# Kernel optimization log

Measured on AMD Instinct MI355X. Metric: run time of the kernel, lower is better.

## Reference

```python
import jax, jax.numpy as jnp
import numpy as np

IN_DIM, HID, MID, FFN, OUT = 384, 128, 1024, 512, 1024
B, T = 8, 4096
LN_EPS = 1e-5


def _legs_hippo(n: int) -> np.ndarray:
    # A[i, j] = P_i(2j/n - 1) * sqrt(2i + 1), Legendre via 3-term recurrence
    x = 2.0 * np.arange(n) / n - 1.0          # eval points, shape [n]
    P = np.zeros((n, n), dtype=np.float64)     # P[i] = P_i(x)
    P[0] = 1.0
    if n > 1:
        P[1] = x
    for i in range(1, n - 1):
        P[i + 1] = ((2 * i + 1) * x * P[i] - i * P[i - 1]) / (i + 1)
    A = P * np.sqrt(2.0 * np.arange(n) + 1.0)[:, None]
    # rescale so the 4096-step recurrence stays finite (A is a free Parameter,
    # so any test value is valid; unscaled LegS overflows fp32 in ~20 steps)
    s = np.linalg.norm(A, 2)
    return (A / (1.05 * s)).astype(np.float32)


def _layernorm(x, g, b):
    mu = jnp.mean(x, axis=-1, keepdims=True)
    var = jnp.var(x, axis=-1, keepdims=True)
    return (x - mu) * jax.lax.rsqrt(var + LN_EPS) * g + b


def setup_inputs() -> dict:
    key = jax.random.key(0)
    ks = jax.random.split(key, 16)

    def w(k, shape, fan_in):
        return jax.random.normal(k, shape, jnp.float32) * (1.0 / np.sqrt(fan_in))

    return {
        "padded_x": jax.random.normal(ks[0], (B, T, IN_DIM), jnp.float32),
        "seq_lens": jax.random.randint(ks[1], (B,), 1, T + 1, jnp.int32),
        "A": jnp.asarray(_legs_hippo(HID)),
        "enc_w1": w(ks[2], (IN_DIM, MID), IN_DIM), "enc_b1": jnp.zeros((MID,), jnp.float32),
        "enc_w2": w(ks[3], (MID, HID), MID), "enc_b2": jnp.zeros((HID,), jnp.float32),
        "proj_w": w(ks[4], (HID, MID), HID), "proj_b": jnp.zeros((MID,), jnp.float32),
        "ln1_g": jnp.ones((MID,), jnp.float32), "ln1_b": jnp.zeros((MID,), jnp.float32),
        "ffn_w1": w(ks[5], (MID, FFN), MID), "ffn_b1": jnp.zeros((FFN,), jnp.float32),
        "ffn_w2": w(ks[6], (FFN, OUT), FFN), "ffn_b2": jnp.zeros((OUT,), jnp.float32),
        "ln2_g": jnp.ones((OUT,), jnp.float32), "ln2_b": jnp.zeros((OUT,), jnp.float32),
        "out_w": w(ks[7], (OUT, OUT), OUT), "out_b": jnp.zeros((OUT,), jnp.float32),
    }


def reference(padded_x, seq_lens, A, enc_w1, enc_b1, enc_w2, enc_b2,
              proj_w, proj_b, ln1_g, ln1_b, ffn_w1, ffn_b1, ffn_w2, ffn_b2,
              ln2_g, ln2_b, out_w, out_b):
    # encoder: Linear -> GELU(exact) -> Linear   [B, T, HID]
    h_mid = jax.nn.gelu(padded_x @ enc_w1 + enc_b1, approximate=False)
    seqs_bx = h_mid @ enc_w2 + enc_b2

    # masked linear recurrence h_t = A @ h_{t-1} + Bx_t via lax.scan over time
    xs = jnp.swapaxes(seqs_bx, 0, 1)           # [T, B, HID]
    ts = jnp.arange(xs.shape[0])

    def step(h, inp):
        x_t, t = inp
        upd = h @ A.T + x_t                     # (A @ h)^T batched
        mask = (t < seq_lens)[:, None]          # [B, 1]
        return jnp.where(mask, upd, h), None

    h0 = jnp.zeros((padded_x.shape[0], A.shape[0]), padded_x.dtype)
    batch_h, _ = jax.lax.scan(step, h0, (xs, ts))

    # decoder
    projected = batch_h @ proj_w + proj_b
    norm_h = _layernorm(projected, ln1_g, ln1_b)
    ffn_out = jax.nn.gelu(norm_h @ ffn_w1 + ffn_b1, approximate=False) @ ffn_w2 + ffn_b2
    ffn_out = ffn_out + projected               # residual (requires OUT == MID)
    norm_ffn = _layernorm(ffn_out, ln2_g, ln2_b)
    return norm_ffn @ out_w + out_b             # [B, OUT]
```

## Files before the change

kernel.cpp:

```cpp
#include <hip/hip_runtime.h>

typedef __attribute__((ext_vector_type(8))) short short8;
typedef __attribute__((ext_vector_type(4))) short short4v;
typedef __attribute__((ext_vector_type(4))) float float4v;

__device__ __forceinline__ float bf2f(short s) {
  union { float f; unsigned u; } cv; cv.u = ((unsigned)(unsigned short)s) << 16; return cv.f;
}
__device__ __forceinline__ short f2bf(float f) {
  union { float f; unsigned u; } cv; cv.f = f;
  unsigned u = cv.u;
  unsigned r = u + 0x7FFFu + ((u >> 16) & 1u);
  return (short)(r >> 16);
}
__device__ __forceinline__ float gelu_f(float v) {
  return 0.5f * v * (1.0f + erff(v * 0.70710678118654752440f));
}
__device__ __forceinline__ void glds16(const short* g, short* l) {
  __builtin_amdgcn_global_load_lds(
      (const __attribute__((address_space(1))) void*)g,
      (__attribute__((address_space(3))) void*)l, 16, 0, 0);
}

template<int EPI>
__global__ __launch_bounds__(256) void gemm_bt(
    const short* __restrict__ A_, const short* __restrict__ BT,
    const float* __restrict__ bias, void* __restrict__ out,
    int lda, int ldb, int ldc, int kSteps, int kChunk,
    const int* __restrict__ seq_lens, int seqSkip)
{
  int m0 = blockIdx.y * 128;
  int n0 = blockIdx.x * 128;
  if (seqSkip) {
    int b = m0 >> 12, t = m0 & 4095;
    if (t >= seq_lens[b]) return;
  }
  int kBase = blockIdx.z * kChunk;

  __shared__ __align__(16) short As[128 * 64];
  __shared__ __align__(16) short Bs[128 * 64];

  int tid = threadIdx.x;
  int lane = tid & 63, wave = tid >> 6;
  int l15 = lane & 15, quad = lane >> 4;
  int wm = wave & 1, wn = wave >> 1;
  int lr = lane >> 3, lseg = lane & 7;

  float4v acc[4][4];
#pragma unroll
  for (int i = 0; i < 4; i++)
#pragma unroll
    for (int j = 0; j < 4; j++) acc[i][j] = 0;

  for (int ks = 0; ks < kSteps; ++ks) {
    int kk = kBase + ks * 64;
#pragma unroll
    for (int i = 0; i < 4; i++) {
      int rowg = wave * 32 + i * 8;
      glds16(A_ + (size_t)(m0 + rowg + lr) * lda + kk + lseg * 8, &As[rowg * 64]);
      glds16(BT + (size_t)(n0 + rowg + lr) * ldb + kk + lseg * 8, &Bs[rowg * 64]);
    }
    __syncthreads();
#pragma unroll
    for (int kh = 0; kh < 2; kh++) {
      short8 af[4], bfr[4];
#pragma unroll
      for (int im = 0; im < 4; im++)
        af[im] = *(short8*)&As[(wm * 64 + im * 16 + l15) * 64 + kh * 32 + quad * 8];
#pragma unroll
      for (int in = 0; in < 4; in++)
        bfr[in] = *(short8*)&Bs[(wn * 64 + in * 16 + l15) * 64 + kh * 32 + quad * 8];
#pragma unroll
      for (int im = 0; im < 4; im++)
#pragma unroll
        for (int in = 0; in < 4; in++)
          acc[im][in] = __builtin_amdgcn_mfma_f32_16x16x32_bf16(af[im], bfr[in], acc[im][in], 0, 0, 0);
    }
    __syncthreads();
  }

#pragma unroll
  for (int im = 0; im < 4; im++) {
#pragma unroll
    for (int in = 0; in < 4; in++) {
      int n = n0 + wn * 64 + in * 16 + l15;
#pragma unroll
      for (int reg = 0; reg < 4; reg++) {
        int m = m0 + wm * 64 + im * 16 + quad * 4 + reg;
        float v = acc[im][in][reg];
        if (EPI == 0) {
          v += bias[n]; v = gelu_f(v);
          ((short*)out)[(size_t)m * ldc + n] = f2bf(v);
        } else if (EPI == 1) {
          v += bias[n];
          ((short*)out)[(size_t)m * ldc + n] = f2bf(v);
        } else {
          atomicAdd((float*)out + (size_t)m * ldc + n, v);
        }
      }
    }
  }
}

__global__ void prep_wide(const float* __restrict__ x, const float* __restrict__ w1,
                          const float* __restrict__ w2,
                          const float* __restrict__ proj_w, const float* __restrict__ ffn_w1,
                          const float* __restrict__ ffn_w2, const float* __restrict__ out_w,
                          const float* __restrict__ A,
                          short* __restrict__ xB,
                          short* __restrict__ w1T, short* __restrict__ w2T,
                          short* __restrict__ projB, short* __restrict__ ffn1B,
                          short* __restrict__ ffn2B, short* __restrict__ outB,
                          short* __restrict__ P1, short* __restrict__ P1t,
                          short* __restrict__ P2t,
                          short* __restrict__ Spow, short* __restrict__ SpowT)
{
  int idx = blockIdx.x * 256 + threadIdx.x;
  if (idx < 3145728) {
    float4v v = ((const float4v*)x)[idx];
    short4v o;
#pragma unroll
    for (int j = 0; j < 4; j++) o[j] = f2bf(v[j]);
    ((short4v*)xB)[idx] = o;
    return;
  }
  idx -= 3145728;
  if (idx < 393216) {
    int n = idx / 384, k = idx % 384;
    w1T[idx] = f2bf(w1[k * 1024 + n]);
    return;
  }
  idx -= 393216;
  if (idx < 131072) {
    int n = idx / 1024, k = idx % 1024;
    w2T[idx] = f2bf(w2[k * 128 + n]);
    return;
  }
  idx -= 131072;
  if (idx < 131072) { projB[idx] = f2bf(proj_w[idx]); return; }
  idx -= 131072;
  if (idx < 524288) { ffn1B[idx] = f2bf(ffn_w1[idx]); return; }
  idx -= 524288;
  if (idx < 524288) { ffn2B[idx] = f2bf(ffn_w2[idx]); return; }
  idx -= 524288;
  if (idx < 1048576) { outB[idx] = f2bf(out_w[idx]); return; }
  idx -= 1048576;
  if (idx < 16384) {
    int i = idx >> 7, j = idx & 127;
    short bidv = f2bf((i == j) ? 1.0f : 0.0f);
    P1[i * 8192 + 63 * 128 + j] = bidv;
    P1t[(63 * 128 + j) * 128 + i] = bidv;
    P2t[(63 * 128 + j) * 128 + i] = bidv;
    short ab = f2bf(A[idx]);
    Spow[idx] = ab;
    SpowT[(size_t)j * 128 + i] = ab;
  }
}

__global__ __launch_bounds__(256) void pow_chain(short* __restrict__ Spow,
                                                 short* __restrict__ SpowT)
{
  __shared__ short X[16384];
  __shared__ short XT[16384];
  int t = threadIdx.x;
  for (int i = t * 8; i < 16384; i += 2048) {
    *(short8*)&X[i]  = *(const short8*)&Spow[i];
    *(short8*)&XT[i] = *(const short8*)&SpowT[i];
  }
  __syncthreads();
  int lane = t & 63, wave = t >> 6, l15 = lane & 15, quad = lane >> 4;
  for (int step = 1; step <= 11; ++step) {
    short8 af[2][4], bfr[8][4];
#pragma unroll
    for (int mt = 0; mt < 2; mt++)
#pragma unroll
      for (int ks = 0; ks < 4; ks++)
        af[mt][ks] = *(short8*)&X[(wave * 32 + mt * 16 + l15) * 128 + ks * 32 + quad * 8];
#pragma unroll
    for (int nt = 0; nt < 8; nt++)
#pragma unroll
      for (int ks = 0; ks < 4; ks++)
        bfr[nt][ks] = *(short8*)&XT[(nt * 16 + l15) * 128 + ks * 32 + quad * 8];
    __syncthreads();
    float4v acc[2][8];
#pragma unroll
    for (int mt = 0; mt < 2; mt++)
#pragma unroll
      for (int nt = 0; nt < 8; nt++) acc[mt][nt] = 0;
#pragma unroll
    for (int ks = 0; ks < 4; ks++)
#pragma unroll
      for (int mt = 0; mt < 2; mt++)
#pragma unroll
        for (int nt = 0; nt < 8; nt++)
          acc[mt][nt] = __builtin_amdgcn_mfma_f32_16x16x32_bf16(af[mt][ks], bfr[nt][ks], acc[mt][nt], 0, 0, 0);
    short* gX  = Spow  + (size_t)step * 16384;
    short* gXT = SpowT + (size_t)step * 16384;
#pragma unroll
    for (int mt = 0; mt < 2; mt++)
#pragma unroll
      for (int nt = 0; nt < 8; nt++)
#pragma unroll
        for (int reg = 0; reg < 4; reg++) {
          int m = wave * 32 + mt * 16 + quad * 4 + reg;
          int n = nt * 16 + l15;
          short v = f2bf(acc[mt][nt][reg]);
          X[m * 128 + n] = v; XT[n * 128 + m] = v;
          gX[m * 128 + n] = v; gXT[n * 128 + m] = v;
        }
    __syncthreads();
  }
}

__global__ __launch_bounds__(256) void pow_fill(const short* __restrict__ Spow,
                                                const short* __restrict__ SpowT,
                                                short* __restrict__ P1,
                                                short* __restrict__ P1t,
                                                short* __restrict__ P2t)
{
  __shared__ short cur[16384];
  __shared__ short Bt[16384];
  int bid = blockIdx.x;
  int table1 = bid < 63;
  int e = table1 ? bid + 1 : bid - 62;
  int t = threadIdx.x;
  int lane = t & 63, wave = t >> 6, l15 = lane & 15, quad = lane >> 4;

  int bits = e;
  int k0 = __ffs(bits) - 1; bits &= bits - 1;
  int s0 = table1 ? k0 : (k0 == 0 ? 6 : 6 + k0);
  for (int i = t * 8; i < 16384; i += 2048)
    *(short8*)&cur[i] = *(const short8*)&Spow[(size_t)s0 * 16384 + i];

  while (bits) {
    int k = __ffs(bits) - 1; bits &= bits - 1;
    int si = table1 ? k : (k == 0 ? 6 : 6 + k);
    for (int i = t * 8; i < 16384; i += 2048)
      *(short8*)&Bt[i] = *(const short8*)&SpowT[(size_t)si * 16384 + i];
    __syncthreads();
    short8 af[2][4], bfr[8][4];
#pragma unroll
    for (int mt = 0; mt < 2; mt++)
#pragma unroll
      for (int ks = 0; ks < 4; ks++)
        af[mt][ks] = *(short8*)&cur[(wave * 32 + mt * 16 + l15) * 128 + ks * 32 + quad * 8];
#pragma unroll
    for (int nt = 0; nt < 8; nt++)
#pragma unroll
      for (int ks = 0; ks < 4; ks++)
        bfr[nt][ks] = *(short8*)&Bt[(nt * 16 + l15) * 128 + ks * 32 + quad * 8];
    __syncthreads();
    float4v acc[2][8];
#pragma unroll
    for (int mt = 0; mt < 2; mt++)
#pragma unroll
      for (int nt = 0; nt < 8; nt++) acc[mt][nt] = 0;
#pragma unroll
    for (int ks = 0; ks < 4; ks++)
#pragma unroll
      for (int mt = 0; mt < 2; mt++)
#pragma unroll
        for (int nt = 0; nt < 8; nt++)
          acc[mt][nt] = __builtin_amdgcn_mfma_f32_16x16x32_bf16(af[mt][ks], bfr[nt][ks], acc[mt][nt], 0, 0, 0);
#pragma unroll
    for (int mt = 0; mt < 2; mt++)
#pragma unroll
      for (int nt = 0; nt < 8; nt++)
#pragma unroll
        for (int reg = 0; reg < 4; reg++) {
          int m = wave * 32 + mt * 16 + quad * 4 + reg;
          int n = nt * 16 + l15;
          cur[m * 128 + n] = f2bf(acc[mt][nt][reg]);
        }
    __syncthreads();
  }
  __syncthreads();
  int slot = 63 - e;
  for (int idx = t; idx < 16384; idx += 256) {
    int i = idx >> 7, j = idx & 127;
    short v = cur[idx];
    if (table1) {
      P1[i * 8192 + slot * 128 + j] = v;
      P1t[(slot * 128 + j) * 128 + i] = v;
    } else {
      P2t[(slot * 128 + j) * 128 + i] = v;
    }
  }
}

__global__ void build_shift(const float* __restrict__ V, const short* __restrict__ seqs,
                            const int* __restrict__ seq_lens,
                            short* __restrict__ Vsh, short* __restrict__ TlX)
{
  int idx = blockIdx.x * 256 + threadIdx.x;
  int pp = idx >> 16;
  int e = idx & 65535;
  int k = e >> 3, b = e & 7;
  int cp = k >> 7, i = k & 127;
  int L = seq_lens[b];
  short v = 0;
  if (pp == 0) {
    int F = L >> 6;
    int sh = 64 - F;
    if (cp >= sh) v = f2bf(V[(size_t)(b * 64 + (cp - sh)) * 128 + i]);
    Vsh[e] = v;
  } else {
    int F = L >> 6, rr = L & 63;
    int sh = 64 - rr;
    if (cp >= sh) v = seqs[((size_t)b * 4096 + F * 64 + (cp - sh)) * 128 + i];
    TlX[e] = v;
  }
}

__global__ __launch_bounds__(256) void tiny_gemm(
    const short* __restrict__ Vsh, const short* __restrict__ TlX,
    const short* __restrict__ P2t, const short* __restrict__ P1t,
    float* __restrict__ hFtail)
{
  int pp = blockIdx.x >> 4, ks = blockIdx.x & 15;
  const short* X = pp ? TlX : Vsh;
  const short* P = pp ? P1t : P2t;
  float* outp = hFtail + pp * 1024;
  int i = threadIdx.x & 127, g = threadIdx.x >> 7;
  float acc[4] = {0, 0, 0, 0};
  for (int k = ks * 512; k < ks * 512 + 512; ++k) {
    float pv = bf2f(P[k * 128 + i]);
    short4v xv = *(const short4v*)(X + k * 8 + g * 4);
#pragma unroll
    for (int q = 0; q < 4; q++) acc[q] += bf2f(xv[q]) * pv;
  }
#pragma unroll
  for (int q = 0; q < 4; q++) atomicAdd(&outp[(g * 4 + q) * 128 + i], acc[q]);
}

__global__ __launch_bounds__(256) void proj_stage(
    const float* __restrict__ hFtail, const short* __restrict__ P1t,
    const int* __restrict__ seq_lens, const short* __restrict__ projB,
    const float* __restrict__ proj_b, float* __restrict__ projected)
{
  __shared__ short hT[128 * 8];
  __shared__ float red[4][64][8];
  int t = threadIdx.x;
  {
    int b = t >> 5, i4 = (t & 31) * 4;
    int rr = seq_lens[b] & 63;
    const short* M = P1t + (size_t)(63 - rr) * 128 * 128;
    const float* hF = hFtail + b * 128;
    float acc[4];
#pragma unroll
    for (int q = 0; q < 4; q++) acc[q] = hFtail[1024 + b * 128 + i4 + q];
    for (int j = 0; j < 128; ++j) {
      float hv = hF[j];
      short4v mv = *(const short4v*)&M[j * 128 + i4];
#pragma unroll
      for (int q = 0; q < 4; q++) acc[q] += bf2f(mv[q]) * hv;
    }
#pragma unroll
    for (int q = 0; q < 4; q++) hT[(i4 + q) * 8 + b] = f2bf(acc[q]);
  }
  __syncthreads();
  int c = t & 63, sl = t >> 6;
  int n = blockIdx.x * 64 + c;
  float acc[8] = {0, 0, 0, 0, 0, 0, 0, 0};
  for (int k = sl * 32; k < sl * 32 + 32; ++k) {
    short8 xv = *(short8*)&hT[k * 8];
    float wv = bf2f(projB[k * 1024 + n]);
#pragma unroll
    for (int b = 0; b < 8; b++) acc[b] += bf2f(xv[b]) * wv;
  }
#pragma unroll
  for (int b = 0; b < 8; b++) red[sl][c][b] = acc[b];
  __syncthreads();
  if (sl == 0) {
#pragma unroll
    for (int s = 1; s < 4; s++)
#pragma unroll
      for (int b = 0; b < 8; b++) acc[b] += red[s][c][b];
    float bn = proj_b[n];
#pragma unroll
    for (int b = 0; b < 8; b++) projected[b * 1024 + n] = acc[b] + bn;
  }
}

__global__ __launch_bounds__(256) void ffn1_stage(
    const float* __restrict__ projected, const float* __restrict__ g1,
    const float* __restrict__ b1, const short* __restrict__ ffn1B,
    float* __restrict__ ffn1raw)
{
  __shared__ float part[8][32][2];
  __shared__ float stats[8][2];
  __shared__ short xT[256 * 8];
  __shared__ float red[4][64][8];
  int t = threadIdx.x;
  { int b = t >> 5, j0 = t & 31; float s = 0, q = 0;
    for (int k = j0 * 32; k < j0 * 32 + 32; ++k) { float v = projected[b * 1024 + k]; s += v; q += v * v; }
    part[b][j0][0] = s; part[b][j0][1] = q; }
  __syncthreads();
  if (t < 8) {
    float s = 0, q = 0;
    for (int j = 0; j < 32; j++) { s += part[t][j][0]; q += part[t][j][1]; }
    float mu = s * (1.0f / 1024.0f);
    float var = q * (1.0f / 1024.0f) - mu * mu;
    stats[t][0] = mu; stats[t][1] = rsqrtf(var + 1e-5f);
  }
  __syncthreads();
  int ky0 = blockIdx.y * 256;
  for (int idx = t; idx < 2048; idx += 256) {
    int kl = idx >> 3, b = idx & 7; int k = ky0 + kl;
    float v = (projected[b * 1024 + k] - stats[b][0]) * stats[b][1] * g1[k] + b1[k];
    xT[kl * 8 + b] = f2bf(v);
  }
  __syncthreads();
  int c = t & 63, sl = t >> 6;
  int n = blockIdx.x * 64 + c;
  float acc[8] = {0, 0, 0, 0, 0, 0, 0, 0};
  for (int kl = sl * 64; kl < sl * 64 + 64; ++kl) {
    short8 xv = *(short8*)&xT[kl * 8];
    float wv = bf2f(ffn1B[(size_t)(ky0 + kl) * 512 + n]);
#pragma unroll
    for (int b = 0; b < 8; b++) acc[b] += bf2f(xv[b]) * wv;
  }
#pragma unroll
  for (int b = 0; b < 8; b++) red[sl][c][b] = acc[b];
  __syncthreads();
  if (sl == 0) {
#pragma unroll
    for (int s = 1; s < 4; s++)
#pragma unroll
      for (int b = 0; b < 8; b++) acc[b] += red[s][c][b];
#pragma unroll
    for (int b = 0; b < 8; b++) atomicAdd(&ffn1raw[b * 512 + n], acc[b]);
  }
}

__global__ __launch_bounds__(256) void ffn2_stage(
    const float* __restrict__ ffn1raw, const float* __restrict__ fb1,
    const short* __restrict__ ffn2B, float* __restrict__ ffn2raw)
{
  __shared__ short xT[256 * 8];
  __shared__ float red[4][64][8];
  int t = threadIdx.x;
  int ky0 = blockIdx.y * 256;
  for (int idx = t; idx < 2048; idx += 256) {
    int kl = idx >> 3, b = idx & 7; int k = ky0 + kl;
    float v = gelu_f(ffn1raw[b * 512 + k] + fb1[k]);
    xT[kl * 8 + b] = f2bf(v);
  }
  __syncthreads();
  int c = t & 63, sl = t >> 6;
  int n = blockIdx.x * 64 + c;
  float acc[8] = {0, 0, 0, 0, 0, 0, 0, 0};
  for (int kl = sl * 64; kl < sl * 64 + 64; ++kl) {
    short8 xv = *(short8*)&xT[kl * 8];
    float wv = bf2f(ffn2B[(size_t)(ky0 + kl) * 1024 + n]);
#pragma unroll
    for (int b = 0; b < 8; b++) acc[b] += bf2f(xv[b]) * wv;
  }
#pragma unroll
  for (int b = 0; b < 8; b++) red[sl][c][b] = acc[b];
  __syncthreads();
  if (sl == 0) {
#pragma unroll
    for (int s = 1; s < 4; s++)
#pragma unroll
      for (int b = 0; b < 8; b++) acc[b] += red[s][c][b];
#pragma unroll
    for (int b = 0; b < 8; b++) atomicAdd(&ffn2raw[b * 1024 + n], acc[b]);
  }
}

__global__ __launch_bounds__(256) void out_stage(
    const float* __restrict__ ffn2raw, const float* __restrict__ fb2,
    const float* __restrict__ projected, const float* __restrict__ g2,
    const float* __restrict__ b2ln, const short* __restrict__ outB,
    const float* __restrict__ out_b, float* __restrict__ d_out)
{
  __shared__ float part[8][32][2];
  __shared__ float stats[8][2];
  __shared__ short xT[512 * 8];
  __shared__ float red[4][64][8];
  int t = threadIdx.x;
  { int b = t >> 5, j0 = t & 31; float s = 0, q = 0;
    for (int k = j0 * 32; k < j0 * 32 + 32; ++k) {
      float v = ffn2raw[b * 1024 + k] + fb2[k] + projected[b * 1024 + k];
      s += v; q += v * v;
    }
    part[b][j0][0] = s; part[b][j0][1] = q; }
  __syncthreads();
  if (t < 8) {
    float s = 0, q = 0;
    for (int j = 0; j < 32; j++) { s += part[t][j][0]; q += part[t][j][1]; }
    float mu = s * (1.0f / 1024.0f);
    float var = q * (1.0f / 1024.0f) - mu * mu;
    stats[t][0] = mu; stats[t][1] = rsqrtf(var + 1e-5f);
  }
  __syncthreads();
  int ky0 = blockIdx.y * 512;
  for (int idx = t; idx < 4096; idx += 256) {
    int kl = idx >> 3, b = idx & 7; int k = ky0 + kl;
    float v = ffn2raw[b * 1024 + k] + fb2[k] + projected[b * 1024 + k];
    v = (v - stats[b][0]) * stats[b][1] * g2[k] + b2ln[k];
    xT[kl * 8 + b] = f2bf(v);
  }
  __syncthreads();
  int c = t & 63, sl = t >> 6;
  int n = blockIdx.x * 64 + c;
  float acc[8] = {0, 0, 0, 0, 0, 0, 0, 0};
  for (int kl = sl * 128; kl < sl * 128 + 128; ++kl) {
    short8 xv = *(short8*)&xT[kl * 8];
    float wv = bf2f(outB[(size_t)(ky0 + kl) * 1024 + n]);
#pragma unroll
    for (int b = 0; b < 8; b++) acc[b] += bf2f(xv[b]) * wv;
  }
#pragma unroll
  for (int b = 0; b < 8; b++) red[sl][c][b] = acc[b];
  __syncthreads();
  if (sl == 0) {
#pragma unroll
    for (int s = 1; s < 4; s++)
#pragma unroll
      for (int b = 0; b < 8; b++) acc[b] += red[s][c][b];
    float bn = (blockIdx.y == 0) ? out_b[n] : 0.0f;
#pragma unroll
    for (int b = 0; b < 8; b++) atomicAdd(&d_out[b * 1024 + n], acc[b] + bn);
  }
}

extern "C" void kernel_launch(void* const* d_in, const int* in_sizes, int n_in,
                              void* d_out, int out_size, void* d_ws, size_t ws_size,
                              hipStream_t stream)
{
  (void)in_sizes; (void)n_in; (void)out_size; (void)ws_size;
  const float* x      = (const float*)d_in[0];
  const int* seq_lens = (const int*)d_in[1];
  const float* A      = (const float*)d_in[2];
  const float* enc_w1 = (const float*)d_in[3];
  const float* enc_b1 = (const float*)d_in[4];
  const float* enc_w2 = (const float*)d_in[5];
  const float* enc_b2 = (const float*)d_in[6];
  const float* proj_w = (const float*)d_in[7];
  const float* proj_b = (const float*)d_in[8];
  const float* ln1_g  = (const float*)d_in[9];
  const float* ln1_b  = (const float*)d_in[10];
  const float* ffn_w1 = (const float*)d_in[11];
  const float* ffn_b1 = (const float*)d_in[12];
  const float* ffn_w2 = (const float*)d_in[13];
  const float* ffn_b2 = (const float*)d_in[14];
  const float* ln2_g  = (const float*)d_in[15];
  const float* ln2_b  = (const float*)d_in[16];
  const float* out_w  = (const float*)d_in[17];
  const float* out_b  = (const float*)d_in[18];

  char* p = (char*)d_ws;
  auto alloc = [&](size_t bytes) { char* r = p; p += (bytes + 255) & ~(size_t)255; return r; };
  short* h_mid = (short*)alloc(32768ull * 1024 * 2);
  short* xB    = (short*)alloc(32768ull * 384 * 2);
  short* seqs  = (short*)alloc(32768ull * 128 * 2);
  short* w1T   = (short*)alloc(1024ull * 384 * 2);
  short* w2T   = (short*)alloc(128ull * 1024 * 2);
  short* projB = (short*)alloc(128ull * 1024 * 2);
  short* ffn1B = (short*)alloc(1024ull * 512 * 2);
  short* ffn2B = (short*)alloc(512ull * 1024 * 2);
  short* outB  = (short*)alloc(1024ull * 1024 * 2);
  short* Spow  = (short*)alloc(12ull * 16384 * 2);
  short* SpowT = (short*)alloc(12ull * 16384 * 2);
  short* P1    = (short*)alloc(128ull * 8192 * 2);
  short* P1t   = (short*)alloc(8192ull * 128 * 2);
  short* P2t   = (short*)alloc(8192ull * 128 * 2);
  float* V       = (float*)alloc(512ull * 128 * 4);
  float* hFtail  = (float*)alloc(2ull * 8 * 128 * 4);
  float* ffn1raw = (float*)alloc(8ull * 512 * 4);
  float* ffn2raw = (float*)alloc(8ull * 1024 * 4);
  short* Vsh   = (short*)alloc(8192ull * 8 * 2);
  short* TlX   = (short*)alloc(8192ull * 8 * 2);
  float* projected = (float*)alloc(8ull * 1024 * 4);

  hipMemsetAsync(V, 0, (512ull * 128 + 2ull * 8 * 128 + 8ull * 512 + 8ull * 1024) * 4, stream);
  hipMemsetAsync(d_out, 0, 8192ull * 4, stream);

  prep_wide<<<23104, 256, 0, stream>>>(x, enc_w1, enc_w2, proj_w, ffn_w1, ffn_w2, out_w, A,
      xB, w1T, w2T, projB, ffn1B, ffn2B, outB, P1, P1t, P2t, Spow, SpowT);
  pow_chain<<<1, 256, 0, stream>>>(Spow, SpowT);
  pow_fill<<<126, 256, 0, stream>>>(Spow, SpowT, P1, P1t, P2t);

  gemm_bt<0><<<dim3(8, 256, 1), 256, 0, stream>>>(xB, w1T, enc_b1, h_mid,
      384, 384, 1024, 6, 0, seq_lens, 1);
  gemm_bt<1><<<dim3(1, 256, 1), 256, 0, stream>>>(h_mid, w2T, enc_b2, seqs,
      1024, 1024, 128, 16, 0, seq_lens, 1);

  gemm_bt<2><<<dim3(1, 4, 16), 256, 0, stream>>>(seqs, P1, nullptr, V,
      8192, 8192, 128, 8, 512, seq_lens, 0);
  build_shift<<<512, 256, 0, stream>>>(V, seqs, seq_lens, Vsh, TlX);
  tiny_gemm<<<32, 256, 0, stream>>>(Vsh, TlX, P2t, P1t, hFtail);

  proj_stage<<<16, 256, 0, stream>>>(hFtail, P1t, seq_lens, projB, proj_b, projected);
  ffn1_stage<<<dim3(8, 4), 256, 0, stream>>>(projected, ln1_g, ln1_b, ffn1B, ffn1raw);
  ffn2_stage<<<dim3(16, 2), 256, 0, stream>>>(ffn1raw, ffn_b1, ffn2B, ffn2raw);
  out_stage<<<dim3(16, 2), 256, 0, stream>>>(ffn2raw, ffn_b2, projected, ln2_g, ln2_b,
      outB, out_b, (float*)d_out);
}
```

Baseline: 441.1 us.

## Fuse encoder GEMMs, swizzle LDS, replace atomics with split-K partials

```diff
diff --git a/kernel.cpp b/kernel.cpp
--- a/kernel.cpp
+++ b/kernel.cpp
@@ -22,19 +22,143 @@
       (__attribute__((address_space(3))) void*)l, 16, 0, 0);
 }
 
-template<int EPI>
+__global__ __launch_bounds__(256) void enc_fused(
+    const short* __restrict__ xB, const short* __restrict__ w1T,
+    const short* __restrict__ w2T, const float* __restrict__ b1,
+    const float* __restrict__ b2, short* __restrict__ seqs,
+    const int* __restrict__ seq_lens)
+{
+  int m0 = blockIdx.x * 64;
+  { int b = m0 >> 12, t = m0 & 4095; if (t >= seq_lens[b]) return; }
+
+  __shared__ __align__(16) short As[64 * 64];
+  __shared__ __align__(16) short Ws[128 * 64];
+  __shared__ __align__(16) short midb[64 * 128];
+
+  int tid = threadIdx.x, lane = tid & 63, wave = tid >> 6;
+  int l15 = lane & 15, quad = lane >> 4;
+  int lr = lane >> 3, lseg = lane & 7;
+
+  float4v accO[4][2];
+#pragma unroll
+  for (int i = 0; i < 4; i++)
+#pragma unroll
+    for (int j = 0; j < 2; j++) accO[i][j] = 0;
+
+  for (int nc = 0; nc < 8; ++nc) {
+    float4v accM[4][2];
+#pragma unroll
+    for (int i = 0; i < 4; i++)
+#pragma unroll
+      for (int j = 0; j < 2; j++) accM[i][j] = 0;
+
+    for (int ks = 0; ks < 6; ++ks) {
+      int kk = ks * 64;
+#pragma unroll
+      for (int i = 0; i < 2; i++) {
+        int rowg = wave * 16 + i * 8;
+        glds16(xB + (size_t)(m0 + rowg + lr) * 384 + kk + (lseg ^ lr) * 8, &As[rowg * 64]);
+      }
+#pragma unroll
+      for (int i = 0; i < 4; i++) {
+        int rowg = wave * 32 + i * 8;
+        glds16(w1T + (size_t)(nc * 128 + rowg + lr) * 384 + kk + (lseg ^ lr) * 8, &Ws[rowg * 64]);
+      }
+      __syncthreads();
+#pragma unroll
+      for (int kh = 0; kh < 2; kh++) {
+        int s = kh * 4 + quad;
+        short8 af[4], bfr[2];
+#pragma unroll
+        for (int im = 0; im < 4; im++) {
+          int r = im * 16 + l15;
+          af[im] = *(short8*)&As[r * 64 + ((s ^ (r & 7)) * 8)];
+        }
+#pragma unroll
+        for (int in = 0; in < 2; in++) {
+          int r = wave * 32 + in * 16 + l15;
+          bfr[in] = *(short8*)&Ws[r * 64 + ((s ^ (r & 7)) * 8)];
+        }
+#pragma unroll
+        for (int im = 0; im < 4; im++)
+#pragma unroll
+          for (int in = 0; in < 2; in++)
+            accM[im][in] = __builtin_amdgcn_mfma_f32_16x16x32_bf16(af[im], bfr[in], accM[im][in], 0, 0, 0);
+      }
+      __syncthreads();
+    }
+#pragma unroll
+    for (int im = 0; im < 4; im++)
+#pragma unroll
+      for (int in = 0; in < 2; in++) {
+        int k = wave * 32 + in * 16 + l15;
+        float bias = b1[nc * 128 + k];
+#pragma unroll
+        for (int reg = 0; reg < 4; reg++) {
+          int m = im * 16 + quad * 4 + reg;
+          float v = gelu_f(accM[im][in][reg] + bias);
+          int s = k >> 3;
+          int sw = (s & 8) | ((s & 7) ^ (m & 7));
+          midb[m * 128 + sw * 8 + (k & 7)] = f2bf(v);
+        }
+      }
+    __syncthreads();
+#pragma unroll
+    for (int ks2 = 0; ks2 < 2; ++ks2) {
+      int kk = nc * 128 + ks2 * 64;
+#pragma unroll
+      for (int i = 0; i < 4; i++) {
+        int rowg = wave * 32 + i * 8;
+        glds16(w2T + (size_t)(rowg + lr) * 1024 + kk + (lseg ^ lr) * 8, &Ws[rowg * 64]);
+      }
+      __syncthreads();
+#pragma unroll
+      for (int kh = 0; kh < 2; kh++) {
+        short8 af[4], bfr[2];
+#pragma unroll
+        for (int im = 0; im < 4; im++) {
+          int m = im * 16 + l15;
+          int kb = ks2 * 64 + kh * 32 + quad * 8;
+          int s = kb >> 3;
+          int sw = (s & 8) | ((s & 7) ^ (m & 7));
+          af[im] = *(short8*)&midb[m * 128 + sw * 8];
+        }
+#pragma unroll
+        for (int in = 0; in < 2; in++) {
+          int r = wave * 32 + in * 16 + l15;
+          int s = kh * 4 + quad;
+          bfr[in] = *(short8*)&Ws[r * 64 + ((s ^ (r & 7)) * 8)];
+        }
+#pragma unroll
+        for (int im = 0; im < 4; im++)
+#pragma unroll
+          for (int in = 0; in < 2; in++)
+            accO[im][in] = __builtin_amdgcn_mfma_f32_16x16x32_bf16(af[im], bfr[in], accO[im][in], 0, 0, 0);
+      }
+      __syncthreads();
+    }
+  }
+#pragma unroll
+  for (int im = 0; im < 4; im++)
+#pragma unroll
+    for (int in = 0; in < 2; in++) {
+      int n = wave * 32 + in * 16 + l15;
+      float bias = b2[n];
+#pragma unroll
+      for (int reg = 0; reg < 4; reg++) {
+        int m = m0 + im * 16 + quad * 4 + reg;
+        seqs[(size_t)m * 128 + n] = f2bf(accO[im][in][reg] + bias);
+      }
+    }
+}
+
 __global__ __launch_bounds__(256) void gemm_bt(
     const short* __restrict__ A_, const short* __restrict__ BT,
-    const float* __restrict__ bias, void* __restrict__ out,
-    int lda, int ldb, int ldc, int kSteps, int kChunk,
-    const int* __restrict__ seq_lens, int seqSkip)
+    float* __restrict__ out, int lda, int ldb, int ldc,
+    int kSteps, int kChunk)
 {
   int m0 = blockIdx.y * 128;
   int n0 = blockIdx.x * 128;
-  if (seqSkip) {
-    int b = m0 >> 12, t = m0 & 4095;
-    if (t >= seq_lens[b]) return;
-  }
   int kBase = blockIdx.z * kChunk;
 
   __shared__ __align__(16) short As[128 * 64];
@@ -57,19 +181,24 @@
 #pragma unroll
     for (int i = 0; i < 4; i++) {
       int rowg = wave * 32 + i * 8;
-      glds16(A_ + (size_t)(m0 + rowg + lr) * lda + kk + lseg * 8, &As[rowg * 64]);
-      glds16(BT + (size_t)(n0 + rowg + lr) * ldb + kk + lseg * 8, &Bs[rowg * 64]);
+      glds16(A_ + (size_t)(m0 + rowg + lr) * lda + kk + (lseg ^ lr) * 8, &As[rowg * 64]);
+      glds16(BT + (size_t)(n0 + rowg + lr) * ldb + kk + (lseg ^ lr) * 8, &Bs[rowg * 64]);
     }
     __syncthreads();
 #pragma unroll
     for (int kh = 0; kh < 2; kh++) {
+      int s = kh * 4 + quad;
       short8 af[4], bfr[4];
 #pragma unroll
-      for (int im = 0; im < 4; im++)
-        af[im] = *(short8*)&As[(wm * 64 + im * 16 + l15) * 64 + kh * 32 + quad * 8];
-#pragma unroll
-      for (int in = 0; in < 4; in++)
-        bfr[in] = *(short8*)&Bs[(wn * 64 + in * 16 + l15) * 64 + kh * 32 + quad * 8];
+      for (int im = 0; im < 4; im++) {
+        int r = wm * 64 + im * 16 + l15;
+        af[im] = *(short8*)&As[r * 64 + ((s ^ (r & 7)) * 8)];
+      }
+#pragma unroll
+      for (int in = 0; in < 4; in++) {
+        int r = wn * 64 + in * 16 + l15;
+        bfr[in] = *(short8*)&Bs[r * 64 + ((s ^ (r & 7)) * 8)];
+      }
 #pragma unroll
       for (int im = 0; im < 4; im++)
 #pragma unroll
@@ -78,28 +207,18 @@
     }
     __syncthreads();
   }
-
-#pragma unroll
-  for (int im = 0; im < 4; im++) {
+  float* outz = out + (size_t)blockIdx.z * 65536;
+#pragma unroll
+  for (int im = 0; im < 4; im++)
 #pragma unroll
     for (int in = 0; in < 4; in++) {
       int n = n0 + wn * 64 + in * 16 + l15;
 #pragma unroll
       for (int reg = 0; reg < 4; reg++) {
         int m = m0 + wm * 64 + im * 16 + quad * 4 + reg;
-        float v = acc[im][in][reg];
-        if (EPI == 0) {
-          v += bias[n]; v = gelu_f(v);
-          ((short*)out)[(size_t)m * ldc + n] = f2bf(v);
-        } else if (EPI == 1) {
-          v += bias[n];
-          ((short*)out)[(size_t)m * ldc + n] = f2bf(v);
-        } else {
-          atomicAdd((float*)out + (size_t)m * ldc + n, v);
-        }
-      }
-    }
-  }
+        outz[(size_t)m * ldc + n] = acc[im][in][reg];
+      }
+    }
 }
 
 __global__ void prep_wide(const float* __restrict__ x, const float* __restrict__ w1,
@@ -288,44 +407,44 @@
   }
 }
 
-__global__ void build_shift(const float* __restrict__ V, const short* __restrict__ seqs,
-                            const int* __restrict__ seq_lens,
-                            short* __restrict__ Vsh, short* __restrict__ TlX)
-{
-  int idx = blockIdx.x * 256 + threadIdx.x;
-  int pp = idx >> 16;
-  int e = idx & 65535;
-  int k = e >> 3, b = e & 7;
-  int cp = k >> 7, i = k & 127;
-  int L = seq_lens[b];
-  short v = 0;
-  if (pp == 0) {
-    int F = L >> 6;
-    int sh = 64 - F;
-    if (cp >= sh) v = f2bf(V[(size_t)(b * 64 + (cp - sh)) * 128 + i]);
-    Vsh[e] = v;
-  } else {
-    int F = L >> 6, rr = L & 63;
-    int sh = 64 - rr;
-    if (cp >= sh) v = seqs[((size_t)b * 4096 + F * 64 + (cp - sh)) * 128 + i];
-    TlX[e] = v;
-  }
-}
-
-__global__ __launch_bounds__(256) void tiny_gemm(
-    const short* __restrict__ Vsh, const short* __restrict__ TlX,
+__global__ __launch_bounds__(256) void combine_gemm(
+    const float* __restrict__ Vz, const short* __restrict__ seqs,
+    const int* __restrict__ seq_lens,
     const short* __restrict__ P2t, const short* __restrict__ P1t,
     float* __restrict__ hFtail)
 {
+  __shared__ short X[512 * 8];
   int pp = blockIdx.x >> 4, ks = blockIdx.x & 15;
-  const short* X = pp ? TlX : Vsh;
+  int t = threadIdx.x;
+  for (int e = t; e < 4096; e += 256) {
+    int klocal = e >> 3, b = e & 7;
+    int cp = ks * 4 + (klocal >> 7), i = klocal & 127;
+    int L = seq_lens[b];
+    if (pp == 0) {
+      int F = L >> 6, sh = 64 - F;
+      float v = 0.f;
+      if (cp >= sh) {
+        int row = (b * 64 + (cp - sh)) * 128 + i;
+#pragma unroll
+        for (int z = 0; z < 16; z++) v += Vz[(size_t)z * 65536 + row];
+      }
+      X[e] = f2bf(v);
+    } else {
+      int F = L >> 6, rr = L & 63, sh = 64 - rr;
+      short s = 0;
+      if (cp >= sh) s = seqs[((size_t)b * 4096 + F * 64 + (cp - sh)) * 128 + i];
+      X[e] = s;
+    }
+  }
+  __syncthreads();
   const short* P = pp ? P1t : P2t;
   float* outp = hFtail + pp * 1024;
-  int i = threadIdx.x & 127, g = threadIdx.x >> 7;
+  int i = t & 127, g = t >> 7;
   float acc[4] = {0, 0, 0, 0};
-  for (int k = ks * 512; k < ks * 512 + 512; ++k) {
+  for (int kl = 0; kl < 512; ++kl) {
+    int k = ks * 512 + kl;
     float pv = bf2f(P[k * 128 + i]);
-    short4v xv = *(const short4v*)(X + k * 8 + g * 4);
+    short4v xv = *(const short4v*)(X + kl * 8 + g * 4);
 #pragma unroll
     for (int q = 0; q < 4; q++) acc[q] += bf2f(xv[q]) * pv;
   }
@@ -553,7 +672,6 @@
 
   char* p = (char*)d_ws;
   auto alloc = [&](size_t bytes) { char* r = p; p += (bytes + 255) & ~(size_t)255; return r; };
-  short* h_mid = (short*)alloc(32768ull * 1024 * 2);
   short* xB    = (short*)alloc(32768ull * 384 * 2);
   short* seqs  = (short*)alloc(32768ull * 128 * 2);
   short* w1T   = (short*)alloc(1024ull * 384 * 2);
@@ -567,15 +685,13 @@
   short* P1    = (short*)alloc(128ull * 8192 * 2);
   short* P1t   = (short*)alloc(8192ull * 128 * 2);
   short* P2t   = (short*)alloc(8192ull * 128 * 2);
-  float* V       = (float*)alloc(512ull * 128 * 4);
+  float* Vz    = (float*)alloc(16ull * 512 * 128 * 4);
   float* hFtail  = (float*)alloc(2ull * 8 * 128 * 4);
   float* ffn1raw = (float*)alloc(8ull * 512 * 4);
   float* ffn2raw = (float*)alloc(8ull * 1024 * 4);
-  short* Vsh   = (short*)alloc(8192ull * 8 * 2);
-  short* TlX   = (short*)alloc(8192ull * 8 * 2);
   float* projected = (float*)alloc(8ull * 1024 * 4);
 
-  hipMemsetAsync(V, 0, (512ull * 128 + 2ull * 8 * 128 + 8ull * 512 + 8ull * 1024) * 4, stream);
+  hipMemsetAsync(hFtail, 0, (2ull * 8 * 128 + 8ull * 512 + 8ull * 1024) * 4, stream);
   hipMemsetAsync(d_out, 0, 8192ull * 4, stream);
 
   prep_wide<<<23104, 256, 0, stream>>>(x, enc_w1, enc_w2, proj_w, ffn_w1, ffn_w2, out_w, A,
@@ -583,15 +699,10 @@
   pow_chain<<<1, 256, 0, stream>>>(Spow, SpowT);
   pow_fill<<<126, 256, 0, stream>>>(Spow, SpowT, P1, P1t, P2t);
 
-  gemm_bt<0><<<dim3(8, 256, 1), 256, 0, stream>>>(xB, w1T, enc_b1, h_mid,
-      384, 384, 1024, 6, 0, seq_lens, 1);
-  gemm_bt<1><<<dim3(1, 256, 1), 256, 0, stream>>>(h_mid, w2T, enc_b2, seqs,
-      1024, 1024, 128, 16, 0, seq_lens, 1);
-
-  gemm_bt<2><<<dim3(1, 4, 16), 256, 0, stream>>>(seqs, P1, nullptr, V,
-      8192, 8192, 128, 8, 512, seq_lens, 0);
-  build_shift<<<512, 256, 0, stream>>>(V, seqs, seq_lens, Vsh, TlX);
-  tiny_gemm<<<32, 256, 0, stream>>>(Vsh, TlX, P2t, P1t, hFtail);
+  enc_fused<<<512, 256, 0, stream>>>(xB, w1T, w2T, enc_b1, enc_b2, seqs, seq_lens);
+
+  gemm_bt<<<dim3(1, 4, 16), 256, 0, stream>>>(seqs, P1, Vz, 8192, 8192, 128, 8, 512);
+  combine_gemm<<<32, 256, 0, stream>>>(Vz, seqs, seq_lens, P2t, P1t, hFtail);
 
   proj_stage<<<16, 256, 0, stream>>>(hFtail, P1t, seq_lens, projB, proj_b, projected);
   ffn1_stage<<<dim3(8, 4), 256, 0, stream>>>(projected, ln1_g, ln1_b, ffn1B, ffn1raw);
```

Measured after the change: 428.9 us. -2.8%, faster.
